# Kernel optimization log

Measured on AMD Instinct MI355X. Metric: run time of the kernel, lower is better.

Reference implementation:

```python
import jax, jax.numpy as jnp
import numpy as np

EPS = 1e-5

def channel_norm(x):
    # per-(batch,channel) norm over spatial dims; torch.var default is unbiased (ddof=1)
    mn = x.mean(axis=(-1, -2), keepdims=True)
    std = jnp.sqrt(x.var(axis=(-1, -2), keepdims=True, ddof=1) + EPS)
    return (x - mn) / std

def conv1x1(x, W, b):
    # x: [B,C,H,W], W: [O,C], b: [O]
    return jnp.einsum('oc,bchw->bohw', W, x) + b[None, :, None, None]

def setup_inputs() -> dict:
    key = jax.random.key(0)
    ks = jax.random.split(key, 10)
    B, C, H, W = 4, 512, 64, 64
    s = 1.0 / np.sqrt(C)  # kaiming-uniform-ish scale for 1x1 conv
    inp = {
        'f_c': jax.random.normal(ks[0], (B, C, H, W), jnp.float32),
        'f_s': jax.random.normal(ks[1], (B, C, H, W), jnp.float32),
        'W_c1': jax.random.uniform(ks[2], (C, C), jnp.float32, -s, s),
        'b_c1': jax.random.uniform(ks[3], (C,), jnp.float32, -s, s),
        'W_s1': jax.random.uniform(ks[4], (C, C), jnp.float32, -s, s),
        'b_s1': jax.random.uniform(ks[5], (C,), jnp.float32, -s, s),
        'W_s2': jax.random.uniform(ks[6], (C, C), jnp.float32, -s, s),
        'b_s2': jax.random.uniform(ks[7], (C,), jnp.float32, -s, s),
        'W_csc': jax.random.uniform(ks[8], (C, C), jnp.float32, -s, s),
        'b_csc': jax.random.uniform(ks[9], (C,), jnp.float32, -s, s),
    }
    return inp

def reference(f_c, f_s, W_c1, b_c1, W_s1, b_s1, W_s2, b_s2, W_csc, b_csc):
    B, C, H, W = f_c.shape
    f_c_hat = channel_norm(f_c)
    f_s_hat = channel_norm(f_s)
    f = conv1x1(f_c_hat, W_c1, b_c1).reshape(B, C, H * W)  # queries [B,C,N]
    g = conv1x1(f_s_hat, W_s1, b_s1).reshape(B, C, H * W)  # keys    [B,C,N]
    scores = jnp.einsum('bci,bcj->bij', f, g)              # [B,N,N]
    attention = jax.nn.softmax(scores, axis=-1)
    h = conv1x1(f_s_hat, W_s2, b_s2).reshape(B, C, H * W)  # values  [B,C,N]
    out = jnp.einsum('bcj,bij->bci', h, attention).reshape(B, C, H, W)
    return conv1x1(out, W_csc, b_csc) + f_c
```

## Files before the change

kernel.cpp:

```cpp
#include <hip/hip_runtime.h>

typedef unsigned short u16;
typedef __attribute__((ext_vector_type(8))) _Float16 f16x8;
typedef __attribute__((ext_vector_type(4))) float f32x4;
typedef __attribute__((ext_vector_type(16))) float f32x16;

#define N_SP 4096
#define C_CH 512
#define B_SZ 4

struct PtrTab { u16* p[4]; };

__device__ __forceinline__ u16 f2h(float f) {
    union { _Float16 h; u16 u; } x; x.h = (_Float16)f; return x.u;
}
__device__ __forceinline__ float h2f(u16 u) {
    union { u16 u; _Float16 h; } x; x.u = u; return (float)x.h;
}
__device__ __forceinline__ void async_cp16(const void* g, void* l) {
    __builtin_amdgcn_global_load_lds((const __attribute__((address_space(1))) unsigned*)g,
                                     (__attribute__((address_space(3))) unsigned*)l, 16, 0, 0);
}
__device__ __forceinline__ float wave_reduce_sum(float v) {
    #pragma unroll
    for (int off = 32; off; off >>= 1) v += __shfl_xor(v, off, 64);
    return v;
}
__device__ __forceinline__ float wave_reduce_max(float v) {
    #pragma unroll
    for (int off = 32; off; off >>= 1) v = fmaxf(v, __shfl_xor(v, off, 64));
    return v;
}
__device__ __forceinline__ void bar() { asm volatile("s_barrier" ::: "memory"); }
template<int N> __device__ __forceinline__ void vmwait() {
    if constexpr (N == 0)  asm volatile("s_waitcnt vmcnt(0)" ::: "memory");
    else if constexpr (N == 2)  asm volatile("s_waitcnt vmcnt(2)" ::: "memory");
    else if constexpr (N == 3)  asm volatile("s_waitcnt vmcnt(3)" ::: "memory");
    else if constexpr (N == 4)  asm volatile("s_waitcnt vmcnt(4)" ::: "memory");
    else if constexpr (N == 6)  asm volatile("s_waitcnt vmcnt(6)" ::: "memory");
    else if constexpr (N == 8)  asm volatile("s_waitcnt vmcnt(8)" ::: "memory");
}

__global__ __launch_bounds__(256) void transpose_cast_stats(
        const float* __restrict__ fc, const float* __restrict__ fs,
        u16* __restrict__ xc, u16* __restrict__ xs,
        float* __restrict__ part_s, float* __restrict__ part_ss) {
    __shared__ float tile[64][65];
    const int t = threadIdx.x;
    const int n0 = blockIdx.x * 64, c0 = blockIdx.y * 64;
    const int z = blockIdx.z;
    const int b = z & 3, which = z >> 2;
    const float* src = which ? fs : fc;
    u16* dst = which ? xs : xc;
    const int r = t >> 4, q4 = (t & 15) * 4;
    #pragma unroll
    for (int it = 0; it < 4; ++it) {
        const int row = it * 16 + r;
        float4 v = *(const float4*)(src + ((size_t)b * C_CH + c0 + row) * N_SP + n0 + q4);
        tile[row][q4 + 0] = v.x; tile[row][q4 + 1] = v.y;
        tile[row][q4 + 2] = v.z; tile[row][q4 + 3] = v.w;
    }
    __syncthreads();
    {
        const int cr = t >> 2, q = t & 3;
        float s = 0.f, ss = 0.f;
        #pragma unroll
        for (int i = 0; i < 16; ++i) {
            float a = tile[cr][q * 16 + i];
            s += a; ss += a * a;
        }
        s += __shfl_xor(s, 1, 64);  s += __shfl_xor(s, 2, 64);
        ss += __shfl_xor(ss, 1, 64); ss += __shfl_xor(ss, 2, 64);
        if (q == 0) {
            atomicAdd(&part_s[z * 512 + c0 + cr], s);
            atomicAdd(&part_ss[z * 512 + c0 + cr], ss);
        }
    }
    #pragma unroll
    for (int it = 0; it < 4; ++it) {
        const int nrow = it * 16 + r;
        ushort4 h4;
        h4.x = f2h(tile[q4 + 0][nrow]);
        h4.y = f2h(tile[q4 + 1][nrow]);
        h4.z = f2h(tile[q4 + 2][nrow]);
        h4.w = f2h(tile[q4 + 3][nrow]);
        *(ushort4*)(dst + ((size_t)b * N_SP + n0 + nrow) * C_CH + c0 + q4) = h4;
    }
}

__global__ __launch_bounds__(256) void prep1(
        const float* __restrict__ W_c1, const float* __restrict__ W_s1,
        const float* __restrict__ W_s2, const float* __restrict__ W_csc,
        const float* __restrict__ b_c1, const float* __restrict__ b_s2,
        const float* __restrict__ b_csc,
        u16* __restrict__ Wbase,
        const float* __restrict__ part_s, const float* __restrict__ part_ss,
        float* __restrict__ mu_a, float* __restrict__ rs_a,
        float* __restrict__ w_u, float* __restrict__ bfold0) {
    __shared__ float tile[64][65];
    const int t = threadIdx.x, z = blockIdx.z;
    if (z < 4) {
        const int n0 = blockIdx.x * 64, c0 = blockIdx.y * 64;
        const float* W = (z == 0) ? W_c1 : (z == 1) ? W_s1 : (z == 2) ? W_s2 : W_csc;
        u16* D = Wbase + ((z == 0) ? 2 : (z == 1) ? 0 : (z == 2) ? 3 : 1) * 262144;
        const int r = t >> 4, q4 = (t & 15) * 4;
        #pragma unroll
        for (int it = 0; it < 4; ++it) {
            const int row = it * 16 + r;
            float4 v = *(const float4*)(W + (size_t)(c0 + row) * 512 + n0 + q4);
            if (z == 3) {
                ushort4 h4 = { f2h(v.x), f2h(v.y), f2h(v.z), f2h(v.w) };
                *(ushort4*)(D + (size_t)(c0 + row) * 512 + n0 + q4) = h4;
            } else {
                tile[row][q4 + 0] = v.x; tile[row][q4 + 1] = v.y;
                tile[row][q4 + 2] = v.z; tile[row][q4 + 3] = v.w;
            }
        }
        __syncthreads();
        if (z == 3) return;
        #pragma unroll
        for (int it = 0; it < 4; ++it) {
            const int nrow = it * 16 + r;
            ushort4 h4;
            h4.x = f2h(tile[q4 + 0][nrow]);
            h4.y = f2h(tile[q4 + 1][nrow]);
            h4.z = f2h(tile[q4 + 2][nrow]);
            h4.w = f2h(tile[q4 + 3][nrow]);
            *(ushort4*)(D + (size_t)(n0 + nrow) * 512 + c0 + q4) = h4;
        }
        return;
    }
    const int flat = blockIdx.y * 8 + blockIdx.x;
    if (flat < 8) {
        #pragma unroll
        for (int h = 0; h < 2; ++h) {
            const int c = flat * 512 + h * 256 + t;
            const float S = part_s[c], SS = part_ss[c];
            const float mean = S * (1.f / N_SP);
            const float var = (SS - S * mean) * (1.f / (N_SP - 1));
            mu_a[c] = mean;
            rs_a[c] = rsqrtf(var + 1e-5f);
        }
    } else if (flat < 10) {
        const int d = (flat - 8) * 256 + t;
        float acc = 0.f;
        for (int o = 0; o < 512; ++o) acc += b_c1[o] * W_s1[(size_t)o * 512 + d];
        w_u[d] = acc;
    } else if (flat < 42) {
        const int w4 = t >> 6, l = t & 63;
        #pragma unroll
        for (int q = 0; q < 4; ++q) {
            const int o = (flat - 10) * 16 + w4 * 4 + q;
            const float4 w0 = *(const float4*)(W_csc + (size_t)o * 512 + l * 8);
            const float4 w1 = *(const float4*)(W_csc + (size_t)o * 512 + l * 8 + 4);
            const float4 b0 = *(const float4*)(b_s2 + l * 8);
            const float4 b1 = *(const float4*)(b_s2 + l * 8 + 4);
            float acc = w0.x * b0.x + w0.y * b0.y + w0.z * b0.z + w0.w * b0.w
                      + w1.x * b1.x + w1.y * b1.y + w1.z * b1.z + w1.w * b1.w;
            acc = wave_reduce_sum(acc);
            if (l == 0) bfold0[o] = acc + b_csc[o];
        }
    }
}

__global__ __launch_bounds__(256) void prep2(
        const u16* __restrict__ WqT16, const u16* __restrict__ Wf16,
        const u16* __restrict__ xs,
        const float* __restrict__ mu_a, const float* __restrict__ rs_a,
        const float* __restrict__ bfold0, const float* __restrict__ w_u,
        u16* __restrict__ Wq_z, u16* __restrict__ Wf_z,
        float* __restrict__ bq, float* __restrict__ bh, float* __restrict__ u_) {
    const int id = blockIdx.x, t = threadIdx.x;
    if (id < 1024) {
        const int y = id >> 9;
        const size_t e = ((size_t)(id & 511) * 256 + t) * 8;
        const int z = (int)(e >> 18), rem = (int)(e & 262143);
        const int d = rem >> 9, a0 = rem & 511;
        u16 v[8];
        if (y == 0) {
            *(uint4*)v = *(const uint4*)(WqT16 + rem);
            const float rd = rs_a[(4 + z) * 512 + d];
            const float* rc = rs_a + z * 512 + a0;
            #pragma unroll
            for (int i = 0; i < 8; ++i) v[i] = f2h(h2f(v[i]) * rc[i] * rd);
            *(uint4*)(Wq_z + e) = *(const uint4*)v;
        } else {
            *(uint4*)v = *(const uint4*)(Wf16 + rem);
            const float* rk = rs_a + (4 + z) * 512 + a0;
            #pragma unroll
            for (int i = 0; i < 8; ++i) v[i] = f2h(h2f(v[i]) * rk[i]);
            *(uint4*)(Wf_z + e) = *(const uint4*)v;
        }
    } else if (id < 2048) {
        const int w = t >> 6, l = t & 63;
        const int oid = (id - 1024) * 4 + w;
        const int kind = oid >> 11;
        const int z = (oid >> 9) & 3, d = oid & 511;
        const u16* row = (kind == 0 ? WqT16 : Wf16) + (size_t)d * 512;
        const int sb = (kind == 0 ? z : 4 + z) * 512;
        float acc = 0.f;
        #pragma unroll
        for (int i = 0; i < 8; ++i) {
            const int a = l * 8 + i;
            acc += h2f(row[a]) * mu_a[sb + a] * rs_a[sb + a];
        }
        acc = wave_reduce_sum(acc);
        if (l == 0) {
            if (kind == 0) bq[z * 512 + d] = -acc * rs_a[(4 + z) * 512 + d];
            else           bh[z * 512 + d] = bfold0[d] - acc;
        }
    } else {
        const int id2 = id - 2048;
        const int b = id2 >> 6, xblk = id2 & 63;
        const int w = t >> 6, l = t & 63;
        float4 u0 = *(const float4*)(w_u + l * 8);
        float4 u1 = *(const float4*)(w_u + l * 8 + 4);
        const float4 r0 = *(const float4*)(rs_a + (4 + b) * 512 + l * 8);
        const float4 r1 = *(const float4*)(rs_a + (4 + b) * 512 + l * 8 + 4);
        u0.x *= r0.x; u0.y *= r0.y; u0.z *= r0.z; u0.w *= r0.w;
        u1.x *= r1.x; u1.y *= r1.y; u1.z *= r1.z; u1.w *= r1.w;
        #pragma unroll
        for (int jj = 0; jj < 16; ++jj) {
            const int j = xblk * 64 + w * 16 + jj;
            const u16* row = xs + ((size_t)b * N_SP + j) * C_CH + l * 8;
            f16x8 x = *(const f16x8*)row;
            float acc = (float)x[0] * u0.x + (float)x[1] * u0.y + (float)x[2] * u0.z + (float)x[3] * u0.w
                      + (float)x[4] * u1.x + (float)x[5] * u1.y + (float)x[6] * u1.z + (float)x[7] * u1.w;
            acc = wave_reduce_sum(acc);
            if (l == 0) u_[(size_t)b * N_SP + j] = acc;
        }
    }
}

enum { OUT_F32 = 0, OUT_F16 = 1 };

template<int OUTMODE, bool TABB, bool TABD, int MI, int MJ>
__global__ __launch_bounds__(256) void gemm_bt(
    const u16* __restrict__ A, const u16* __restrict__ B, PtrTab tab,
    float* __restrict__ Df, u16* __restrict__ Dh,
    const float* __restrict__ bias_m, const float* __restrict__ bias_n,
    const float* __restrict__ res,
    int M, int N, int K, int lda, int ldb, int ldd,
    size_t sA, size_t sB, size_t sD, size_t sR, int sBm, int sBn)
{
    constexpr int TM = MI * 64, TN = MJ * 64, BK = 64;
    constexpr int AITS = (TM * BK) / (256 * 8);
    constexpr int BITS = (TN * BK) / (256 * 8);
    __shared__ u16 smem[(TM + TN) * BK];
    u16* As = smem;
    u16* Bs = smem + TM * BK;

    const int t = threadIdx.x;
    const int l = t & 63, w = t >> 6;
    const int m0 = blockIdx.y * TM, n0 = blockIdx.x * TN;
    const size_t zb = blockIdx.z;
    const u16* pA = A + zb * sA + (size_t)m0 * lda;
    const u16* pB = (TABB ? tab.p[zb] : B + zb * sB) + (size_t)n0 * ldb;

    const int wr = (w & 1) * (MI * 32), wc = (w >> 1) * (MJ * 32);

    f32x16 acc[MI][MJ] = {};

    for (int k0 = 0; k0 < K; k0 += BK) {
        #pragma unroll
        for (int it = 0; it < AITS; ++it) {
            const int L = it * 256 + t;
            const int row = L >> 3, c = L & 7;
            const int sc = (c ^ (row & 7)) * 8;
            async_cp16(pA + (size_t)row * lda + k0 + sc, As + L * 8);
        }
        #pragma unroll
        for (int it = 0; it < BITS; ++it) {
            const int L = it * 256 + t;
            const int row = L >> 3, c = L & 7;
            const int sc = (c ^ (row & 7)) * 8;
            async_cp16(pB + (size_t)row * ldb + k0 + sc, Bs + L * 8);
        }
        __syncthreads();
        #pragma unroll
        for (int kk = 0; kk < 4; ++kk) {
            f16x8 af[MI], bf[MJ];
            #pragma unroll
            for (int i = 0; i < MI; ++i) {
                const int row = wr + i * 32 + (l & 31);
                const int ch = ((kk * 2 + (l >> 5)) ^ (row & 7)) * 8;
                af[i] = *(const f16x8*)(As + row * BK + ch);
            }
            #pragma unroll
            for (int j = 0; j < MJ; ++j) {
                const int row = wc + j * 32 + (l & 31);
                const int ch = ((kk * 2 + (l >> 5)) ^ (row & 7)) * 8;
                bf[j] = *(const f16x8*)(Bs + row * BK + ch);
            }
            #pragma unroll
            for (int i = 0; i < MI; ++i)
                #pragma unroll
                for (int j = 0; j < MJ; ++j)
                    acc[i][j] = __builtin_amdgcn_mfma_f32_32x32x16_f16(af[i], bf[j], acc[i][j], 0, 0, 0);
        }
        __syncthreads();
    }

    const int cl = l & 31, rh = (l >> 5) * 4;
    u16* pDh = (OUTMODE == OUT_F16) ? (TABD ? tab.p[zb] : Dh + zb * sD) : nullptr;
    float* pDf = (OUTMODE == OUT_F32) ? (Df + zb * sD) : nullptr;
    #pragma unroll
    for (int i = 0; i < MI; ++i) {
        #pragma unroll
        for (int j = 0; j < MJ; ++j) {
            const int nn = n0 + wc + j * 32 + cl;
            const float bn = bias_n ? bias_n[(size_t)sBn * zb + nn] : 0.f;
            #pragma unroll
            for (int reg = 0; reg < 16; ++reg) {
                const int ml = (reg & 3) + 8 * (reg >> 2) + rh;
                const int mm = m0 + wr + i * 32 + ml;
                float v = acc[i][j][reg] + bn;
                if (bias_m) v += bias_m[(size_t)sBm * zb + mm];
                const size_t off = (size_t)mm * ldd + nn;
                if (OUTMODE == OUT_F32) {
                    if (res) v += res[zb * sR + off];
                    pDf[off] = v;
                } else {
                    pDh[off] = f2h(v);
                }
            }
        }
    }
}

template<int OUTMODE, bool TABB, bool TABD, int BM>
__global__ __launch_bounds__(512, 2) void gemm_p16(
    const u16* __restrict__ A, const u16* __restrict__ B, PtrTab tab,
    float* __restrict__ Df, u16* __restrict__ Dh,
    const float* __restrict__ bias_m, const float* __restrict__ bias_n,
    const float* __restrict__ res,
    int K, int lda, int ldb, int ldd,
    size_t sA, size_t sB, size_t sD, size_t sR, int sBm, int sBn)
{
    constexpr int BN = 256, BK = 64;
    constexpr int HM = BM / 2;
    constexpr int MF = BM / 64;
    constexpr int LA = BM / 128;
    constexpr int LB = 2;
    constexpr int LDSH = (BM + BN) * BK;
    __shared__ u16 smem[2 * LDSH];

    const int t = threadIdx.x;
    const int l = t & 63, w = t >> 6;
    const int m0 = blockIdx.y * BM, n0 = blockIdx.x * BN;
    const size_t zb = blockIdx.z;
    const u16* pA = A + zb * sA + (size_t)m0 * lda;
    const u16* pB = (TABB ? tab.p[zb] : B + zb * sB) + (size_t)n0 * ldb;

    const int wr = (w & 1) * (HM / 2);
    const int wc = (w >> 1) * 32;

    f32x4 acc[2 * MF][4] = {};

    auto stageA = [&](int buf, int k0, int half) {
        u16* dst = smem + buf * LDSH;
        #pragma unroll
        for (int it = 0; it < LA; ++it) {
            const int L = it * 512 + t;
            const int row = half * HM + (L >> 3), c = L & 7;
            const int cs = c ^ (((row >> 2) & 1) << 1);
            async_cp16(pA + (size_t)row * lda + k0 + cs * 8, dst + row * BK + c * 8);
        }
    };
    auto stageB = [&](int buf, int k0, int half) {
        u16* dst = smem + buf * LDSH + BM * BK;
        #pragma unroll
        for (int it = 0; it < LB; ++it) {
            const int L = it * 512 + t;
            const int row = half * 128 + (L >> 3), c = L & 7;
            const int cs = c ^ (((row >> 2) & 1) << 1);
            async_cp16(pB + (size_t)row * ldb + k0 + cs * 8, dst + row * BK + c * 8);
        }
    };
    auto rdA = [&](const u16* As, int qi, int mf, int kk) -> f16x8 {
        const int row = qi * HM + wr + mf * 16 + (l & 15);
        const int ch = (kk * 4 + (l >> 4)) ^ (((row >> 2) & 1) << 1);
        return *(const f16x8*)(As + row * BK + ch * 8);
    };
    auto rdB = [&](const u16* Bs, int qj, int nf, int kk) -> f16x8 {
        const int row = qj * 128 + wc + nf * 16 + (l & 15);
        const int ch = (kk * 4 + (l >> 4)) ^ (((row >> 2) & 1) << 1);
        return *(const f16x8*)(Bs + row * BK + ch * 8);
    };

    const int NT = K / BK;
    stageA(0, 0, 0); stageB(0, 0, 0); stageA(0, 0, 1); stageB(0, 0, 1);

    f16x8 af[MF][2], bf[2][2];

    for (int tl = 0; tl < NT; ++tl) {
        const int cur = tl & 1, nxt = cur ^ 1;
        const u16* As = smem + cur * LDSH;
        const u16* Bs = As + BM * BK;
        const int k1 = (tl + 1) * BK;
        const bool pf = (tl + 1 < NT);

        vmwait<LA + LB>();
        bar();
        #pragma unroll
        for (int mf = 0; mf < MF; ++mf) {
            af[mf][0] = rdA(As, 0, mf, 0); af[mf][1] = rdA(As, 0, mf, 1);
        }
        #pragma unroll
        for (int nf = 0; nf < 2; ++nf) {
            bf[nf][0] = rdB(Bs, 0, nf, 0); bf[nf][1] = rdB(Bs, 0, nf, 1);
        }
        if (pf) stageA(nxt, k1, 0);
        asm volatile("s_waitcnt lgkmcnt(0)" ::: "memory");
        __builtin_amdgcn_sched_barrier(0);
        __builtin_amdgcn_s_setprio(1);
        #pragma unroll
        for (int mf = 0; mf < MF; ++mf)
            #pragma unroll
            for (int nf = 0; nf < 2; ++nf) {
                acc[mf][nf] = __builtin_amdgcn_mfma_f32_16x16x32_f16(af[mf][0], bf[nf][0], acc[mf][nf], 0, 0, 0);
                acc[mf][nf] = __builtin_amdgcn_mfma_f32_16x16x32_f16(af[mf][1], bf[nf][1], acc[mf][nf], 0, 0, 0);
            }
        __builtin_amdgcn_s_setprio(0);

        if (pf) vmwait<LA + LB>(); else vmwait<LB>();
        bar();
        #pragma unroll
        for (int mf = 0; mf < MF; ++mf) {
            af[mf][0] = rdA(As, 1, mf, 0); af[mf][1] = rdA(As, 1, mf, 1);
        }
        if (pf) stageB(nxt, k1, 0);
        asm volatile("s_waitcnt lgkmcnt(0)" ::: "memory");
        __builtin_amdgcn_sched_barrier(0);
        __builtin_amdgcn_s_setprio(1);
        #pragma unroll
        for (int mf = 0; mf < MF; ++mf)
            #pragma unroll
            for (int nf = 0; nf < 2; ++nf) {
                acc[MF + mf][nf] = __builtin_amdgcn_mfma_f32_16x16x32_f16(af[mf][0], bf[nf][0], acc[MF + mf][nf], 0, 0, 0);
                acc[MF + mf][nf] = __builtin_amdgcn_mfma_f32_16x16x32_f16(af[mf][1], bf[nf][1], acc[MF + mf][nf], 0, 0, 0);
            }
        __builtin_amdgcn_s_setprio(0);

        if (pf) vmwait<LA + LB>(); else vmwait<0>();
        bar();
        #pragma unroll
        for (int nf = 0; nf < 2; ++nf) {
            bf[nf][0] = rdB(Bs, 1, nf, 0); bf[nf][1] = rdB(Bs, 1, nf, 1);
        }
        if (pf) stageA(nxt, k1, 1);
        asm volatile("s_waitcnt lgkmcnt(0)" ::: "memory");
        __builtin_amdgcn_sched_barrier(0);
        __builtin_amdgcn_s_setprio(1);
        #pragma unroll
        for (int mf = 0; mf < MF; ++mf)
            #pragma unroll
            for (int nf = 0; nf < 2; ++nf) {
                acc[MF + mf][2 + nf] = __builtin_amdgcn_mfma_f32_16x16x32_f16(af[mf][0], bf[nf][0], acc[MF + mf][2 + nf], 0, 0, 0);
                acc[MF + mf][2 + nf] = __builtin_amdgcn_mfma_f32_16x16x32_f16(af[mf][1], bf[nf][1], acc[MF + mf][2 + nf], 0, 0, 0);
            }
        __builtin_amdgcn_s_setprio(0);

        bar();
        #pragma unroll
        for (int mf = 0; mf < MF; ++mf) {
            af[mf][0] = rdA(As, 0, mf, 0); af[mf][1] = rdA(As, 0, mf, 1);
        }
        if (pf) stageB(nxt, k1, 1);
        asm volatile("s_waitcnt lgkmcnt(0)" ::: "memory");
        __builtin_amdgcn_sched_barrier(0);
        __builtin_amdgcn_s_setprio(1);
        #pragma unroll
        for (int mf = 0; mf < MF; ++mf)
            #pragma unroll
            for (int nf = 0; nf < 2; ++nf) {
                acc[mf][2 + nf] = __builtin_amdgcn_mfma_f32_16x16x32_f16(af[mf][0], bf[nf][0], acc[mf][2 + nf], 0, 0, 0);
                acc[mf][2 + nf] = __builtin_amdgcn_mfma_f32_16x16x32_f16(af[mf][1], bf[nf][1], acc[mf][2 + nf], 0, 0, 0);
            }
        __builtin_amdgcn_s_setprio(0);
    }

    const int cl = l & 15, rh = (l >> 4) * 4;
    u16* pDh = (OUTMODE == OUT_F16) ? (TABD ? tab.p[zb] : Dh + zb * sD) : nullptr;
    float* pDf = (OUTMODE == OUT_F32) ? (Df + zb * sD) : nullptr;
    #pragma unroll
    for (int qi = 0; qi < 2; ++qi) {
        #pragma unroll
        for (int qj = 0; qj < 2; ++qj) {
            #pragma unroll
            for (int mf = 0; mf < MF; ++mf) {
                #pragma unroll
                for (int nf = 0; nf < 2; ++nf) {
                    const int nn = n0 + qj * 128 + wc + nf * 16 + cl;
                    const float bn = bias_n ? bias_n[(size_t)sBn * zb + nn] : 0.f;
                    const f32x4 a4 = acc[qi * MF + mf][qj * 2 + nf];
                    #pragma unroll
                    for (int reg = 0; reg < 4; ++reg) {
                        const int mm = m0 + qi * HM + wr + mf * 16 + rh + reg;
                        float v = a4[reg] + bn;
                        if (bias_m) v += bias_m[(size_t)sBm * zb + mm];
                        const size_t off = (size_t)mm * ldd + nn;
                        if (OUTMODE == OUT_F32) {
                            if (res) v += res[zb * sR + off];
                            pDf[off] = v;
                        } else {
                            pDh[off] = f2h(v);
                        }
                    }
                }
            }
        }
    }
}

__global__ __launch_bounds__(256) void softmax_kernel(PtrTab tab) {
    u16* row = tab.p[blockIdx.y] + (size_t)blockIdx.x * N_SP;
    const int t = threadIdx.x;
    u16 raw[16];
    *(uint4*)(raw + 0) = *(const uint4*)(row + t * 16);
    *(uint4*)(raw + 8) = *(const uint4*)(row + t * 16 + 8);
    float v[16];
    float mx = -1e30f;
    #pragma unroll
    for (int i = 0; i < 16; ++i) { v[i] = h2f(raw[i]); mx = fmaxf(mx, v[i]); }
    mx = wave_reduce_max(mx);
    __shared__ float red[4];
    const int wave = t >> 6;
    if ((t & 63) == 0) red[wave] = mx;
    __syncthreads();
    mx = fmaxf(fmaxf(red[0], red[1]), fmaxf(red[2], red[3]));
    float sum = 0.f;
    #pragma unroll
    for (int i = 0; i < 16; ++i) { v[i] = __expf(v[i] - mx); sum += v[i]; }
    sum = wave_reduce_sum(sum);
    __syncthreads();
    if ((t & 63) == 0) red[wave] = sum;
    __syncthreads();
    const float inv = 1.f / (red[0] + red[1] + red[2] + red[3]);
    #pragma unroll
    for (int i = 0; i < 16; ++i) raw[i] = f2h(v[i] * inv);
    *(uint4*)(row + t * 16)     = *(const uint4*)(raw + 0);
    *(uint4*)(row + t * 16 + 8) = *(const uint4*)(raw + 8);
}

extern "C" void kernel_launch(void* const* d_in, const int* in_sizes, int n_in,
                              void* d_out, int out_size, void* d_ws, size_t ws_size,
                              hipStream_t stream) {
    const float* f_c   = (const float*)d_in[0];
    const float* f_s   = (const float*)d_in[1];
    const float* W_c1  = (const float*)d_in[2];
    const float* b_c1  = (const float*)d_in[3];
    const float* W_s1  = (const float*)d_in[4];
    const float* b_s1  = (const float*)d_in[5]; (void)b_s1;
    const float* W_s2  = (const float*)d_in[6];
    const float* b_s2  = (const float*)d_in[7];
    const float* W_csc = (const float*)d_in[8];
    const float* b_csc = (const float*)d_in[9];

    const size_t PB = (size_t)N_SP * C_CH;
    const size_t M1 = 1024 * 1024;

    u16* ws   = (u16*)d_ws;
    u16* Xs   = ws;
    u16* q_   = ws + 8 * M1;
    u16* hc   = ws + 16 * M1;
    u16* Xc   = ws + 24 * M1;
    u16* S3   = ws + 24 * M1;
    u16* S0   = ws + 40 * M1;
    u16* S1   = ws + 56 * M1;
    u16* S2   = ws + 72 * M1;
    u16* Wbase= ws + 88 * M1;
    u16* WqT16= Wbase + 4 * 262144;
    u16* Wf16 = Wbase + 5 * 262144;
    u16* Wq_z = Wbase + 6 * 262144;
    u16* Wf_z = Wq_z + 1048576;
    float* f32b = (float*)(ws + 92 * M1);
    float* part_s  = f32b;
    float* part_ss = f32b + 4096;
    float* mu_a    = f32b + 8192;
    float* rs_a    = f32b + 12288;
    float* w_u     = f32b + 16384;
    float* bfold0  = f32b + 16896;
    float* bq      = f32b + 17408;
    float* bh      = f32b + 19456;
    float* u_      = f32b + 21504;

    PtrTab Stab; Stab.p[0] = S0; Stab.p[1] = S1; Stab.p[2] = S2; Stab.p[3] = S3;
    PtrTab tab0 = Stab;

    hipMemsetAsync(part_s, 0, 2 * 4096 * sizeof(float), stream);

    transpose_cast_stats<<<dim3(64, 8, 8), 256, 0, stream>>>(f_c, f_s, Xc, Xs, part_s, part_ss);

    prep1<<<dim3(8, 8, 5), 256, 0, stream>>>(W_c1, W_s1, W_s2, W_csc, b_c1, b_s2, b_csc,
                                             Wbase, part_s, part_ss, mu_a, rs_a, w_u, bfold0);

    gemm_bt<OUT_F16, false, false, 2, 2><<<dim3(4, 4, 2), 256, 0, stream>>>(
        Wbase, Wbase + 2 * 262144, tab0, nullptr, WqT16, nullptr, nullptr, nullptr,
        512, 512, 512, 512, 512, 512, 262144, 262144, 262144, 0, 0, 0);

    prep2<<<2304, 256, 0, stream>>>(WqT16, Wf16, Xs, mu_a, rs_a, bfold0, w_u,
                                    Wq_z, Wf_z, bq, bh, u_);

    gemm_p16<OUT_F16, false, false, 128><<<dim3(2, 32, B_SZ), 512, 0, stream>>>(
        Xc, Wq_z, tab0, nullptr, q_, nullptr, bq, nullptr,
        C_CH, C_CH, C_CH, C_CH, PB, 262144, PB, 0, 0, 512);
    gemm_p16<OUT_F16, false, false, 128><<<dim3(16, 4, B_SZ), 512, 0, stream>>>(
        Wf_z, Xs, tab0, nullptr, hc, bh, nullptr, nullptr,
        C_CH, C_CH, C_CH, N_SP, 262144, PB, PB, 0, 512, 0);

    gemm_p16<OUT_F16, false, true, 256><<<dim3(16, 16, B_SZ), 512, 0, stream>>>(
        q_, Xs, Stab, nullptr, nullptr, nullptr, u_, nullptr,
        C_CH, C_CH, C_CH, N_SP, PB, PB, 0, 0, 0, N_SP);

    softmax_kernel<<<dim3(N_SP, B_SZ), 256, 0, stream>>>(Stab);

    gemm_p16<OUT_F32, true, false, 128><<<dim3(16, 4, B_SZ), 512, 0, stream>>>(
        hc, nullptr, Stab, (float*)d_out, nullptr, nullptr, nullptr, f_c,
        N_SP, N_SP, N_SP, N_SP, PB, 0, PB, PB, 0, 0);
}
```

Before: 446.1 us.

## Replace async global-to-LDS copies with register-staged loads and padded LDS rows

Changes the main fp16 MFMA GEMM to load the next K-tile from global memory into registers and write it to LDS later, instead of using direct async global_load_lds copies. The XOR swizzle is replaced by row padding (stride BK+8) to avoid LDS bank conflicts. It also reorders the four quadrant MFMA phases so the A and B LDS writes land in different phases. This costs extra VGPRs and LDS capacity, which may reduce occupancy under the 512x2 launch bound, and adds explicit LDS write instructions.

```diff
diff --git a/kernel.cpp b/kernel.cpp
--- a/kernel.cpp
+++ b/kernel.cpp
@@ -35,10 +35,13 @@
 template<int N> __device__ __forceinline__ void vmwait() {
     if constexpr (N == 0)  asm volatile("s_waitcnt vmcnt(0)" ::: "memory");
     else if constexpr (N == 2)  asm volatile("s_waitcnt vmcnt(2)" ::: "memory");
-    else if constexpr (N == 3)  asm volatile("s_waitcnt vmcnt(3)" ::: "memory");
     else if constexpr (N == 4)  asm volatile("s_waitcnt vmcnt(4)" ::: "memory");
     else if constexpr (N == 6)  asm volatile("s_waitcnt vmcnt(6)" ::: "memory");
     else if constexpr (N == 8)  asm volatile("s_waitcnt vmcnt(8)" ::: "memory");
+}
+__device__ __forceinline__ void lgkm0() {
+    asm volatile("s_waitcnt lgkmcnt(0)" ::: "memory");
+    __builtin_amdgcn_sched_barrier(0);
 }
 
 __global__ __launch_bounds__(256) void transpose_cast_stats(
@@ -329,7 +332,7 @@
 }
 
 template<int OUTMODE, bool TABB, bool TABD, int BM>
-__global__ __launch_bounds__(512, 2) void gemm_p16(
+__global__ __launch_bounds__(512, 2) void gemm_rs(
     const u16* __restrict__ A, const u16* __restrict__ B, PtrTab tab,
     float* __restrict__ Df, u16* __restrict__ Dh,
     const float* __restrict__ bias_m, const float* __restrict__ bias_n,
@@ -337,13 +340,13 @@
     int K, int lda, int ldb, int ldd,
     size_t sA, size_t sB, size_t sD, size_t sR, int sBm, int sBn)
 {
-    constexpr int BN = 256, BK = 64;
+    constexpr int BN = 256, BK = 64, RS = BK + 8;
     constexpr int HM = BM / 2;
     constexpr int MF = BM / 64;
-    constexpr int LA = BM / 128;
-    constexpr int LB = 2;
-    constexpr int LDSH = (BM + BN) * BK;
-    __shared__ u16 smem[2 * LDSH];
+    constexpr int GA = BM / 64;
+    constexpr int GB = BN / 64;
+    constexpr int BUF = (BM + BN) * RS;
+    __shared__ u16 smem[2 * BUF];
 
     const int t = threadIdx.x;
     const int l = t & 63, w = t >> 6;
@@ -356,63 +359,71 @@
     const int wc = (w >> 1) * 32;
 
     f32x4 acc[2 * MF][4] = {};
-
-    auto stageA = [&](int buf, int k0, int half) {
-        u16* dst = smem + buf * LDSH;
-        #pragma unroll
-        for (int it = 0; it < LA; ++it) {
-            const int L = it * 512 + t;
-            const int row = half * HM + (L >> 3), c = L & 7;
-            const int cs = c ^ (((row >> 2) & 1) << 1);
-            async_cp16(pA + (size_t)row * lda + k0 + cs * 8, dst + row * BK + c * 8);
+    uint4 rg[GA + GB];
+
+    auto gloadA = [&](int k0) {
+        #pragma unroll
+        for (int i = 0; i < GA; ++i) {
+            const int L = i * 512 + t, row = L >> 3, c = L & 7;
+            rg[i] = *(const uint4*)(pA + (size_t)row * lda + k0 + c * 8);
         }
     };
-    auto stageB = [&](int buf, int k0, int half) {
-        u16* dst = smem + buf * LDSH + BM * BK;
-        #pragma unroll
-        for (int it = 0; it < LB; ++it) {
-            const int L = it * 512 + t;
-            const int row = half * 128 + (L >> 3), c = L & 7;
-            const int cs = c ^ (((row >> 2) & 1) << 1);
-            async_cp16(pB + (size_t)row * ldb + k0 + cs * 8, dst + row * BK + c * 8);
+    auto gloadB = [&](int k0) {
+        #pragma unroll
+        for (int i = 0; i < GB; ++i) {
+            const int L = i * 512 + t, row = L >> 3, c = L & 7;
+            rg[GA + i] = *(const uint4*)(pB + (size_t)row * ldb + k0 + c * 8);
+        }
+    };
+    auto wldsA = [&](int buf) {
+        u16* dA = smem + buf * BUF;
+        #pragma unroll
+        for (int i = 0; i < GA; ++i) {
+            const int L = i * 512 + t, row = L >> 3, c = L & 7;
+            *(uint4*)(dA + row * RS + c * 8) = rg[i];
+        }
+    };
+    auto wldsB = [&](int buf) {
+        u16* dB = smem + buf * BUF + BM * RS;
+        #pragma unroll
+        for (int i = 0; i < GB; ++i) {
+            const int L = i * 512 + t, row = L >> 3, c = L & 7;
+            *(uint4*)(dB + row * RS + c * 8) = rg[GA + i];
         }
     };
     auto rdA = [&](const u16* As, int qi, int mf, int kk) -> f16x8 {
         const int row = qi * HM + wr + mf * 16 + (l & 15);
-        const int ch = (kk * 4 + (l >> 4)) ^ (((row >> 2) & 1) << 1);
-        return *(const f16x8*)(As + row * BK + ch * 8);
+        const int ch = kk * 4 + (l >> 4);
+        return *(const f16x8*)(As + row * RS + ch * 8);
     };
     auto rdB = [&](const u16* Bs, int qj, int nf, int kk) -> f16x8 {
         const int row = qj * 128 + wc + nf * 16 + (l & 15);
-        const int ch = (kk * 4 + (l >> 4)) ^ (((row >> 2) & 1) << 1);
-        return *(const f16x8*)(Bs + row * BK + ch * 8);
+        const int ch = kk * 4 + (l >> 4);
+        return *(const f16x8*)(Bs + row * RS + ch * 8);
     };
 
+    f16x8 af[MF][2], bf[2][2];
+
     const int NT = K / BK;
-    stageA(0, 0, 0); stageB(0, 0, 0); stageA(0, 0, 1); stageB(0, 0, 1);
-
-    f16x8 af[MF][2], bf[2][2];
+    gloadA(0); gloadB(0);
+    vmwait<0>();
+    wldsA(0); wldsB(0);
+    lgkm0();
+    bar();
 
     for (int tl = 0; tl < NT; ++tl) {
         const int cur = tl & 1, nxt = cur ^ 1;
-        const u16* As = smem + cur * LDSH;
-        const u16* Bs = As + BM * BK;
+        const u16* As = smem + cur * BUF;
+        const u16* Bs = As + BM * RS;
         const int k1 = (tl + 1) * BK;
         const bool pf = (tl + 1 < NT);
 
-        vmwait<LA + LB>();
-        bar();
-        #pragma unroll
-        for (int mf = 0; mf < MF; ++mf) {
-            af[mf][0] = rdA(As, 0, mf, 0); af[mf][1] = rdA(As, 0, mf, 1);
-        }
-        #pragma unroll
-        for (int nf = 0; nf < 2; ++nf) {
-            bf[nf][0] = rdB(Bs, 0, nf, 0); bf[nf][1] = rdB(Bs, 0, nf, 1);
-        }
-        if (pf) stageA(nxt, k1, 0);
-        asm volatile("s_waitcnt lgkmcnt(0)" ::: "memory");
-        __builtin_amdgcn_sched_barrier(0);
+        #pragma unroll
+        for (int mf = 0; mf < MF; ++mf) { af[mf][0] = rdA(As, 0, mf, 0); af[mf][1] = rdA(As, 0, mf, 1); }
+        #pragma unroll
+        for (int nf = 0; nf < 2; ++nf) { bf[nf][0] = rdB(Bs, 0, nf, 0); bf[nf][1] = rdB(Bs, 0, nf, 1); }
+        if (pf) { gloadA(k1); gloadB(k1); }
+        lgkm0();
         __builtin_amdgcn_s_setprio(1);
         #pragma unroll
         for (int mf = 0; mf < MF; ++mf)
@@ -422,16 +433,41 @@
                 acc[mf][nf] = __builtin_amdgcn_mfma_f32_16x16x32_f16(af[mf][1], bf[nf][1], acc[mf][nf], 0, 0, 0);
             }
         __builtin_amdgcn_s_setprio(0);
-
-        if (pf) vmwait<LA + LB>(); else vmwait<LB>();
         bar();
-        #pragma unroll
-        for (int mf = 0; mf < MF; ++mf) {
-            af[mf][0] = rdA(As, 1, mf, 0); af[mf][1] = rdA(As, 1, mf, 1);
-        }
-        if (pf) stageB(nxt, k1, 0);
-        asm volatile("s_waitcnt lgkmcnt(0)" ::: "memory");
-        __builtin_amdgcn_sched_barrier(0);
+
+        #pragma unroll
+        for (int nf = 0; nf < 2; ++nf) { bf[nf][0] = rdB(Bs, 1, nf, 0); bf[nf][1] = rdB(Bs, 1, nf, 1); }
+        lgkm0();
+        __builtin_amdgcn_s_setprio(1);
+        #pragma unroll
+        for (int mf = 0; mf < MF; ++mf)
+            #pragma unroll
+            for (int nf = 0; nf < 2; ++nf) {
+                acc[mf][2 + nf] = __builtin_amdgcn_mfma_f32_16x16x32_f16(af[mf][0], bf[nf][0], acc[mf][2 + nf], 0, 0, 0);
+                acc[mf][2 + nf] = __builtin_amdgcn_mfma_f32_16x16x32_f16(af[mf][1], bf[nf][1], acc[mf][2 + nf], 0, 0, 0);
+            }
+        __builtin_amdgcn_s_setprio(0);
+        bar();
+
+        #pragma unroll
+        for (int mf = 0; mf < MF; ++mf) { af[mf][0] = rdA(As, 1, mf, 0); af[mf][1] = rdA(As, 1, mf, 1); }
+        if (pf) { vmwait<GB>(); wldsA(nxt); }
+        lgkm0();
+        __builtin_amdgcn_s_setprio(1);
+        #pragma unroll
+        for (int mf = 0; mf < MF; ++mf)
+            #pragma unroll
+            for (int nf = 0; nf < 2; ++nf) {
+                acc[MF + mf][2 + nf] = __builtin_amdgcn_mfma_f32_16x16x32_f16(af[mf][0], bf[nf][0], acc[MF + mf][2 + nf], 0, 0, 0);
+                acc[MF + mf][2 + nf] = __builtin_amdgcn_mfma_f32_16x16x32_f16(af[mf][1], bf[nf][1], acc[MF + mf][2 + nf], 0, 0, 0);
+            }
+        __builtin_amdgcn_s_setprio(0);
+        bar();
+
+        #pragma unroll
+        for (int nf = 0; nf < 2; ++nf) { bf[nf][0] = rdB(Bs, 0, nf, 0); bf[nf][1] = rdB(Bs, 0, nf, 1); }
+        if (pf) { vmwait<0>(); wldsB(nxt); }
+        lgkm0();
         __builtin_amdgcn_s_setprio(1);
         #pragma unroll
         for (int mf = 0; mf < MF; ++mf)
@@ -441,43 +477,7 @@
                 acc[MF + mf][nf] = __builtin_amdgcn_mfma_f32_16x16x32_f16(af[mf][1], bf[nf][1], acc[MF + mf][nf], 0, 0, 0);
             }
         __builtin_amdgcn_s_setprio(0);
-
-        if (pf) vmwait<LA + LB>(); else vmwait<0>();
         bar();
-        #pragma unroll
-        for (int nf = 0; nf < 2; ++nf) {
-            bf[nf][0] = rdB(Bs, 1, nf, 0); bf[nf][1] = rdB(Bs, 1, nf, 1);
-        }
-        if (pf) stageA(nxt, k1, 1);
-        asm volatile("s_waitcnt lgkmcnt(0)" ::: "memory");
-        __builtin_amdgcn_sched_barrier(0);
-        __builtin_amdgcn_s_setprio(1);
-        #pragma unroll
-        for (int mf = 0; mf < MF; ++mf)
-            #pragma unroll
-            for (int nf = 0; nf < 2; ++nf) {
-                acc[MF + mf][2 + nf] = __builtin_amdgcn_mfma_f32_16x16x32_f16(af[mf][0], bf[nf][0], acc[MF + mf][2 + nf], 0, 0, 0);
-                acc[MF + mf][2 + nf] = __builtin_amdgcn_mfma_f32_16x16x32_f16(af[mf][1], bf[nf][1], acc[MF + mf][2 + nf], 0, 0, 0);
-            }
-        __builtin_amdgcn_s_setprio(0);
-
-        bar();
-        #pragma unroll
-        for (int mf = 0; mf < MF; ++mf) {
-            af[mf][0] = rdA(As, 0, mf, 0); af[mf][1] = rdA(As, 0, mf, 1);
-        }
-        if (pf) stageB(nxt, k1, 1);
-        asm volatile("s_waitcnt lgkmcnt(0)" ::: "memory");
-        __builtin_amdgcn_sched_barrier(0);
-        __builtin_amdgcn_s_setprio(1);
-        #pragma unroll
-        for (int mf = 0; mf < MF; ++mf)
-            #pragma unroll
-            for (int nf = 0; nf < 2; ++nf) {
-                acc[mf][2 + nf] = __builtin_amdgcn_mfma_f32_16x16x32_f16(af[mf][0], bf[nf][0], acc[mf][2 + nf], 0, 0, 0);
-                acc[mf][2 + nf] = __builtin_amdgcn_mfma_f32_16x16x32_f16(af[mf][1], bf[nf][1], acc[mf][2 + nf], 0, 0, 0);
-            }
-        __builtin_amdgcn_s_setprio(0);
     }
 
     const int cl = l & 15, rh = (l >> 4) * 4;
@@ -602,20 +602,20 @@
     prep2<<<2304, 256, 0, stream>>>(WqT16, Wf16, Xs, mu_a, rs_a, bfold0, w_u,
                                     Wq_z, Wf_z, bq, bh, u_);
 
-    gemm_p16<OUT_F16, false, false, 128><<<dim3(2, 32, B_SZ), 512, 0, stream>>>(
+    gemm_rs<OUT_F16, false, false, 128><<<dim3(2, 32, B_SZ), 512, 0, stream>>>(
         Xc, Wq_z, tab0, nullptr, q_, nullptr, bq, nullptr,
         C_CH, C_CH, C_CH, C_CH, PB, 262144, PB, 0, 0, 512);
-    gemm_p16<OUT_F16, false, false, 128><<<dim3(16, 4, B_SZ), 512, 0, stream>>>(
+    gemm_rs<OUT_F16, false, false, 128><<<dim3(16, 4, B_SZ), 512, 0, stream>>>(
         Wf_z, Xs, tab0, nullptr, hc, bh, nullptr, nullptr,
         C_CH, C_CH, C_CH, N_SP, 262144, PB, PB, 0, 512, 0);
 
-    gemm_p16<OUT_F16, false, true, 256><<<dim3(16, 16, B_SZ), 512, 0, stream>>>(
+    gemm_rs<OUT_F16, false, true, 256><<<dim3(16, 16, B_SZ), 512, 0, stream>>>(
         q_, Xs, Stab, nullptr, nullptr, nullptr, u_, nullptr,
         C_CH, C_CH, C_CH, N_SP, PB, PB, 0, 0, 0, N_SP);
 
     softmax_kernel<<<dim3(N_SP, B_SZ), 256, 0, stream>>>(Stab);
 
-    gemm_p16<OUT_F32, true, false, 128><<<dim3(16, 4, B_SZ), 512, 0, stream>>>(
+    gemm_rs<OUT_F32, true, false, 128><<<dim3(16, 4, B_SZ), 512, 0, stream>>>(
         hc, nullptr, Stab, (float*)d_out, nullptr, nullptr, nullptr, f_c,
         N_SP, N_SP, N_SP, N_SP, PB, 0, PB, PB, 0, 0);
 }
```

New measurement: 651.9 us. 46.1% more time.

## Restructure GEMM pipeline with full XOR swizzle and reordered quadrant staging

Applied to the files above, without the earlier changes.

Rewrites the main GEMM loop so A-fragments for both M halves stay in registers, reordering quadrant compute and async loads so fewer barriers and waits sit on the critical path. It changes the LDS swizzle from a 2-bit XOR to a full row&7 XOR to cut bank conflicts on fragment reads. It also moves the scores GEMM from 256-row to 128-row tiles, giving more blocks. Holding extra fragment registers may raise register pressure at two blocks per CU.

```diff
diff --git a/kernel.cpp b/kernel.cpp
--- a/kernel.cpp
+++ b/kernel.cpp
@@ -35,10 +35,13 @@
 template<int N> __device__ __forceinline__ void vmwait() {
     if constexpr (N == 0)  asm volatile("s_waitcnt vmcnt(0)" ::: "memory");
     else if constexpr (N == 2)  asm volatile("s_waitcnt vmcnt(2)" ::: "memory");
-    else if constexpr (N == 3)  asm volatile("s_waitcnt vmcnt(3)" ::: "memory");
     else if constexpr (N == 4)  asm volatile("s_waitcnt vmcnt(4)" ::: "memory");
     else if constexpr (N == 6)  asm volatile("s_waitcnt vmcnt(6)" ::: "memory");
     else if constexpr (N == 8)  asm volatile("s_waitcnt vmcnt(8)" ::: "memory");
+}
+__device__ __forceinline__ void lgkm0() {
+    asm volatile("s_waitcnt lgkmcnt(0)" ::: "memory");
+    __builtin_amdgcn_sched_barrier(0);
 }
 
 __global__ __launch_bounds__(256) void transpose_cast_stats(
@@ -329,7 +332,7 @@
 }
 
 template<int OUTMODE, bool TABB, bool TABD, int BM>
-__global__ __launch_bounds__(512, 2) void gemm_p16(
+__global__ __launch_bounds__(512, 2) void gemm_f(
     const u16* __restrict__ A, const u16* __restrict__ B, PtrTab tab,
     float* __restrict__ Df, u16* __restrict__ Dh,
     const float* __restrict__ bias_m, const float* __restrict__ bias_n,
@@ -363,8 +366,8 @@
         for (int it = 0; it < LA; ++it) {
             const int L = it * 512 + t;
             const int row = half * HM + (L >> 3), c = L & 7;
-            const int cs = c ^ (((row >> 2) & 1) << 1);
-            async_cp16(pA + (size_t)row * lda + k0 + cs * 8, dst + row * BK + c * 8);
+            const int sc = (c ^ (row & 7)) * 8;
+            async_cp16(pA + (size_t)row * lda + k0 + sc, dst + row * BK + c * 8);
         }
     };
     auto stageB = [&](int buf, int k0, int half) {
@@ -373,25 +376,28 @@
         for (int it = 0; it < LB; ++it) {
             const int L = it * 512 + t;
             const int row = half * 128 + (L >> 3), c = L & 7;
-            const int cs = c ^ (((row >> 2) & 1) << 1);
-            async_cp16(pB + (size_t)row * ldb + k0 + cs * 8, dst + row * BK + c * 8);
+            const int sc = (c ^ (row & 7)) * 8;
+            async_cp16(pB + (size_t)row * ldb + k0 + sc, dst + row * BK + c * 8);
         }
     };
     auto rdA = [&](const u16* As, int qi, int mf, int kk) -> f16x8 {
         const int row = qi * HM + wr + mf * 16 + (l & 15);
-        const int ch = (kk * 4 + (l >> 4)) ^ (((row >> 2) & 1) << 1);
+        const int ch = (kk * 4 + (l >> 4)) ^ (row & 7);
         return *(const f16x8*)(As + row * BK + ch * 8);
     };
     auto rdB = [&](const u16* Bs, int qj, int nf, int kk) -> f16x8 {
         const int row = qj * 128 + wc + nf * 16 + (l & 15);
-        const int ch = (kk * 4 + (l >> 4)) ^ (((row >> 2) & 1) << 1);
+        const int ch = (kk * 4 + (l >> 4)) ^ (row & 7);
         return *(const f16x8*)(Bs + row * BK + ch * 8);
     };
 
+    f16x8 af[2][MF][2];
+    f16x8 bf[2][2];
+
     const int NT = K / BK;
-    stageA(0, 0, 0); stageB(0, 0, 0); stageA(0, 0, 1); stageB(0, 0, 1);
-
-    f16x8 af[MF][2], bf[2][2];
+    stageA(0, 0, 0); stageA(0, 0, 1); stageB(0, 0, 0); stageB(0, 0, 1);
+    vmwait<LB>();
+    bar();
 
     for (int tl = 0; tl < NT; ++tl) {
         const int cur = tl & 1, nxt = cur ^ 1;
@@ -400,84 +406,66 @@
         const int k1 = (tl + 1) * BK;
         const bool pf = (tl + 1 < NT);
 
-        vmwait<LA + LB>();
+        #pragma unroll
+        for (int mf = 0; mf < MF; ++mf) { af[0][mf][0] = rdA(As, 0, mf, 0); af[0][mf][1] = rdA(As, 0, mf, 1); }
+        #pragma unroll
+        for (int nf = 0; nf < 2; ++nf) { bf[nf][0] = rdB(Bs, 0, nf, 0); bf[nf][1] = rdB(Bs, 0, nf, 1); }
+        if (pf) stageA(nxt, k1, 0);
+        lgkm0();
+        __builtin_amdgcn_s_setprio(1);
+        #pragma unroll
+        for (int mf = 0; mf < MF; ++mf)
+            #pragma unroll
+            for (int nf = 0; nf < 2; ++nf) {
+                acc[mf][nf] = __builtin_amdgcn_mfma_f32_16x16x32_f16(af[0][mf][0], bf[nf][0], acc[mf][nf], 0, 0, 0);
+                acc[mf][nf] = __builtin_amdgcn_mfma_f32_16x16x32_f16(af[0][mf][1], bf[nf][1], acc[mf][nf], 0, 0, 0);
+            }
+        __builtin_amdgcn_s_setprio(0);
         bar();
-        #pragma unroll
-        for (int mf = 0; mf < MF; ++mf) {
-            af[mf][0] = rdA(As, 0, mf, 0); af[mf][1] = rdA(As, 0, mf, 1);
-        }
-        #pragma unroll
-        for (int nf = 0; nf < 2; ++nf) {
-            bf[nf][0] = rdB(Bs, 0, nf, 0); bf[nf][1] = rdB(Bs, 0, nf, 1);
-        }
-        if (pf) stageA(nxt, k1, 0);
-        asm volatile("s_waitcnt lgkmcnt(0)" ::: "memory");
-        __builtin_amdgcn_sched_barrier(0);
+
+        #pragma unroll
+        for (int mf = 0; mf < MF; ++mf) { af[1][mf][0] = rdA(As, 1, mf, 0); af[1][mf][1] = rdA(As, 1, mf, 1); }
+        if (pf) stageA(nxt, k1, 1);
+        lgkm0();
         __builtin_amdgcn_s_setprio(1);
         #pragma unroll
         for (int mf = 0; mf < MF; ++mf)
             #pragma unroll
             for (int nf = 0; nf < 2; ++nf) {
-                acc[mf][nf] = __builtin_amdgcn_mfma_f32_16x16x32_f16(af[mf][0], bf[nf][0], acc[mf][nf], 0, 0, 0);
-                acc[mf][nf] = __builtin_amdgcn_mfma_f32_16x16x32_f16(af[mf][1], bf[nf][1], acc[mf][nf], 0, 0, 0);
+                acc[MF + mf][nf] = __builtin_amdgcn_mfma_f32_16x16x32_f16(af[1][mf][0], bf[nf][0], acc[MF + mf][nf], 0, 0, 0);
+                acc[MF + mf][nf] = __builtin_amdgcn_mfma_f32_16x16x32_f16(af[1][mf][1], bf[nf][1], acc[MF + mf][nf], 0, 0, 0);
             }
         __builtin_amdgcn_s_setprio(0);
-
-        if (pf) vmwait<LA + LB>(); else vmwait<LB>();
+        if (pf) vmwait<2 * LA>(); else vmwait<0>();
         bar();
-        #pragma unroll
-        for (int mf = 0; mf < MF; ++mf) {
-            af[mf][0] = rdA(As, 1, mf, 0); af[mf][1] = rdA(As, 1, mf, 1);
-        }
+
+        #pragma unroll
+        for (int nf = 0; nf < 2; ++nf) { bf[nf][0] = rdB(Bs, 1, nf, 0); bf[nf][1] = rdB(Bs, 1, nf, 1); }
         if (pf) stageB(nxt, k1, 0);
-        asm volatile("s_waitcnt lgkmcnt(0)" ::: "memory");
-        __builtin_amdgcn_sched_barrier(0);
+        lgkm0();
         __builtin_amdgcn_s_setprio(1);
         #pragma unroll
         for (int mf = 0; mf < MF; ++mf)
             #pragma unroll
             for (int nf = 0; nf < 2; ++nf) {
-                acc[MF + mf][nf] = __builtin_amdgcn_mfma_f32_16x16x32_f16(af[mf][0], bf[nf][0], acc[MF + mf][nf], 0, 0, 0);
-                acc[MF + mf][nf] = __builtin_amdgcn_mfma_f32_16x16x32_f16(af[mf][1], bf[nf][1], acc[MF + mf][nf], 0, 0, 0);
+                acc[MF + mf][2 + nf] = __builtin_amdgcn_mfma_f32_16x16x32_f16(af[1][mf][0], bf[nf][0], acc[MF + mf][2 + nf], 0, 0, 0);
+                acc[MF + mf][2 + nf] = __builtin_amdgcn_mfma_f32_16x16x32_f16(af[1][mf][1], bf[nf][1], acc[MF + mf][2 + nf], 0, 0, 0);
             }
         __builtin_amdgcn_s_setprio(0);
-
-        if (pf) vmwait<LA + LB>(); else vmwait<0>();
         bar();
-        #pragma unroll
-        for (int nf = 0; nf < 2; ++nf) {
-            bf[nf][0] = rdB(Bs, 1, nf, 0); bf[nf][1] = rdB(Bs, 1, nf, 1);
-        }
-        if (pf) stageA(nxt, k1, 1);
-        asm volatile("s_waitcnt lgkmcnt(0)" ::: "memory");
-        __builtin_amdgcn_sched_barrier(0);
+
+        if (pf) stageB(nxt, k1, 1);
         __builtin_amdgcn_s_setprio(1);
         #pragma unroll
         for (int mf = 0; mf < MF; ++mf)
             #pragma unroll
             for (int nf = 0; nf < 2; ++nf) {
-                acc[MF + mf][2 + nf] = __builtin_amdgcn_mfma_f32_16x16x32_f16(af[mf][0], bf[nf][0], acc[MF + mf][2 + nf], 0, 0, 0);
-                acc[MF + mf][2 + nf] = __builtin_amdgcn_mfma_f32_16x16x32_f16(af[mf][1], bf[nf][1], acc[MF + mf][2 + nf], 0, 0, 0);
+                acc[mf][2 + nf] = __builtin_amdgcn_mfma_f32_16x16x32_f16(af[0][mf][0], bf[nf][0], acc[mf][2 + nf], 0, 0, 0);
+                acc[mf][2 + nf] = __builtin_amdgcn_mfma_f32_16x16x32_f16(af[0][mf][1], bf[nf][1], acc[mf][2 + nf], 0, 0, 0);
             }
         __builtin_amdgcn_s_setprio(0);
-
+        if (pf) vmwait<LB>();
         bar();
-        #pragma unroll
-        for (int mf = 0; mf < MF; ++mf) {
-            af[mf][0] = rdA(As, 0, mf, 0); af[mf][1] = rdA(As, 0, mf, 1);
-        }
-        if (pf) stageB(nxt, k1, 1);
-        asm volatile("s_waitcnt lgkmcnt(0)" ::: "memory");
-        __builtin_amdgcn_sched_barrier(0);
-        __builtin_amdgcn_s_setprio(1);
-        #pragma unroll
-        for (int mf = 0; mf < MF; ++mf)
-            #pragma unroll
-            for (int nf = 0; nf < 2; ++nf) {
-                acc[mf][2 + nf] = __builtin_amdgcn_mfma_f32_16x16x32_f16(af[mf][0], bf[nf][0], acc[mf][2 + nf], 0, 0, 0);
-                acc[mf][2 + nf] = __builtin_amdgcn_mfma_f32_16x16x32_f16(af[mf][1], bf[nf][1], acc[mf][2 + nf], 0, 0, 0);
-            }
-        __builtin_amdgcn_s_setprio(0);
     }
 
     const int cl = l & 15, rh = (l >> 4) * 4;
@@ -602,20 +590,20 @@
     prep2<<<2304, 256, 0, stream>>>(WqT16, Wf16, Xs, mu_a, rs_a, bfold0, w_u,
                                     Wq_z, Wf_z, bq, bh, u_);
 
-    gemm_p16<OUT_F16, false, false, 128><<<dim3(2, 32, B_SZ), 512, 0, stream>>>(
+    gemm_f<OUT_F16, false, false, 128><<<dim3(2, 32, B_SZ), 512, 0, stream>>>(
         Xc, Wq_z, tab0, nullptr, q_, nullptr, bq, nullptr,
         C_CH, C_CH, C_CH, C_CH, PB, 262144, PB, 0, 0, 512);
-    gemm_p16<OUT_F16, false, false, 128><<<dim3(16, 4, B_SZ), 512, 0, stream>>>(
+    gemm_f<OUT_F16, false, false, 128><<<dim3(16, 4, B_SZ), 512, 0, stream>>>(
         Wf_z, Xs, tab0, nullptr, hc, bh, nullptr, nullptr,
         C_CH, C_CH, C_CH, N_SP, 262144, PB, PB, 0, 512, 0);
 
-    gemm_p16<OUT_F16, false, true, 256><<<dim3(16, 16, B_SZ), 512, 0, stream>>>(
+    gemm_f<OUT_F16, false, true, 128><<<dim3(16, 32, B_SZ), 512, 0, stream>>>(
         q_, Xs, Stab, nullptr, nullptr, nullptr, u_, nullptr,
         C_CH, C_CH, C_CH, N_SP, PB, PB, 0, 0, 0, N_SP);
 
     softmax_kernel<<<dim3(N_SP, B_SZ), 256, 0, stream>>>(Stab);
 
-    gemm_p16<OUT_F32, true, false, 128><<<dim3(16, 4, B_SZ), 512, 0, stream>>>(
+    gemm_f<OUT_F32, true, false, 128><<<dim3(16, 4, B_SZ), 512, 0, stream>>>(
         hc, nullptr, Stab, (float*)d_out, nullptr, nullptr, nullptr, f_c,
         N_SP, N_SP, N_SP, N_SP, PB, 0, PB, PB, 0, 0);
 }
```

Result: no change. 448.5 us (+0.5%).
